# Kernel tuning notes

Measured on AMD Instinct MI355X. Metric: run time of the kernel, lower is better.

The kernel has to match this reference:

```python
import jax, jax.numpy as jnp
import numpy as np

EPS = 1e-5

def _bn(x, g, b):
    # training-mode BatchNorm1d over the batch axis (axis 0), biased variance
    m = jnp.mean(x, axis=0)
    v = jnp.var(x, axis=0)
    return g * (x - m) / jnp.sqrt(v + EPS) + b

def _mlp(x, w1, b1, g1, be1, w2, b2, g2, be2, w3, b3):
    # Linear -> BN -> ReLU -> Linear -> BN -> ReLU -> Linear
    x = jax.nn.relu(_bn(x @ w1.T + b1, g1, be1))
    x = jax.nn.relu(_bn(x @ w2.T + b2, g2, be2))
    return x @ w3.T + b3

def setup_inputs() -> dict:
    key = jax.random.key(0)
    ks = jax.random.split(key, 10)
    B, S, D = 256, 512, 128
    w = lambda k: jax.random.normal(k, (D, D), jnp.float32) * 0.05
    return {
        "s": jax.random.normal(ks[0], (B, S, D), jnp.float32),
        "c": jax.random.normal(ks[1], (B, D), jnp.float32),
        "s_w1": w(ks[2]), "s_b1": jnp.zeros((D,), jnp.float32),
        "s_g1": jnp.ones((D,), jnp.float32), "s_be1": jnp.zeros((D,), jnp.float32),
        "s_w2": w(ks[3]), "s_b2": jnp.zeros((D,), jnp.float32),
        "s_g2": jnp.ones((D,), jnp.float32), "s_be2": jnp.zeros((D,), jnp.float32),
        "s_w3": w(ks[4]), "s_b3": jnp.zeros((D,), jnp.float32),
        "c_w1": w(ks[5]), "c_b1": jnp.zeros((D,), jnp.float32),
        "c_g1": jnp.ones((D,), jnp.float32), "c_be1": jnp.zeros((D,), jnp.float32),
        "c_w2": w(ks[6]), "c_b2": jnp.zeros((D,), jnp.float32),
        "c_g2": jnp.ones((D,), jnp.float32), "c_be2": jnp.zeros((D,), jnp.float32),
        "c_w3": w(ks[7]), "c_b3": jnp.zeros((D,), jnp.float32),
    }

def reference(s, c,
              s_w1, s_b1, s_g1, s_be1, s_w2, s_b2, s_g2, s_be2, s_w3, s_b3,
              c_w1, c_b1, c_g1, c_be1, c_w2, c_b2, c_g2, c_be2, c_w3, c_b3):
    # c_mlp: [B, D] -> [B, D] (BN over batch)
    c_out = _mlp(c, c_w1, c_b1, c_g1, c_be1, c_w2, c_b2, c_g2, c_be2, c_w3, c_b3)
    # s_mlp applied per sequence slice; BN stats over batch axis 0 only
    # (matches the torch loop where each s[:, i, :] gets its own BN stats).
    # s: [B, S, D]; _bn with axis=0 gives per-(slice, feature) stats.
    s_h = _mlp(s, s_w1, s_b1, s_g1, s_be1, s_w2, s_b2, s_g2, s_be2, s_w3, s_b3)
    s_out = s_h * c_out[:, None, :]          # context gate, [B, S, D]
    aggregated_c = jnp.max(s_out, axis=1)    # pooling == 'max', [B, D]
    return (s_out, aggregated_c)
```

## Files before the change

kernel.cpp:

```cpp
#include <hip/hip_runtime.h>
#include <hip/hip_bf16.h>
#include <math.h>

#define BATCH 256
#define SEQ   512
#define DIM   128
#define LDSK  136
#define LDSF  132

typedef __attribute__((ext_vector_type(8))) __bf16  bf16x8;
typedef __attribute__((ext_vector_type(4))) __bf16  bf16x4;
typedef __attribute__((ext_vector_type(4))) float   f32x4;

template<int RT>
__device__ __forceinline__ void matmul_layer(
    const __bf16* __restrict__ Xa, const __bf16* __restrict__ wg,
    const float* bias, f32x4 (&acc)[RT][8], int wave, int m, int q)
{
  const int rowbase = wave * RT * 16;
#pragma unroll
  for (int ct = 0; ct < 8; ++ct) {
    const float b = bias[ct * 16 + m];
    const f32x4 bv = {b, b, b, b};
#pragma unroll
    for (int rt = 0; rt < RT; ++rt) acc[rt][ct] = bv;
  }
#pragma unroll
  for (int ks = 0; ks < 4; ++ks) {
    const int k0 = ks * 32 + q * 8;
    bf16x8 a[RT], bw[8];
#pragma unroll
    for (int rt = 0; rt < RT; ++rt)
      a[rt] = *(const bf16x8*)(Xa + (rowbase + rt * 16 + m) * LDSK + k0);
#pragma unroll
    for (int ct = 0; ct < 8; ++ct)
      bw[ct] = *(const bf16x8*)(wg + (ct * 16 + m) * DIM + k0);
#pragma unroll
    for (int rt = 0; rt < RT; ++rt)
#pragma unroll
      for (int ct = 0; ct < 8; ++ct)
        acc[rt][ct] = __builtin_amdgcn_mfma_f32_16x16x32_bf16(a[rt], bw[ct], acc[rt][ct], 0, 0, 0);
  }
}

template<int RT>
__device__ __forceinline__ void stats_accum(
    const f32x4 (&acc)[RT][8], float* sumL, float* sqL, int m, int q)
{
#pragma unroll
  for (int ct = 0; ct < 8; ++ct) {
    float s = 0.f, ss = 0.f;
#pragma unroll
    for (int rt = 0; rt < RT; ++rt)
#pragma unroll
      for (int r = 0; r < 4; ++r) { const float v = acc[rt][ct][r]; s += v; ss += v * v; }
    s  += __shfl_xor(s, 16, 64);  s  += __shfl_xor(s, 32, 64);
    ss += __shfl_xor(ss, 16, 64); ss += __shfl_xor(ss, 32, 64);
    if (q == 0) { atomicAdd(&sumL[ct * 16 + m], s); atomicAdd(&sqL[ct * 16 + m], ss); }
  }
}

template<int RT>
__device__ __forceinline__ void bn_relu_store(
    const f32x4 (&acc)[RT][8], __bf16* Xa, const float* sumL, const float* sqL,
    const float* g, const float* be, int wave, int m, int q)
{
  const int rowbase = wave * RT * 16;
#pragma unroll
  for (int ct = 0; ct < 8; ++ct) {
    const int n = ct * 16 + m;
    const float mean = sumL[n] * (1.0f / BATCH);
    const float var  = sqL[n]  * (1.0f / BATCH) - mean * mean;
    const float a = g[n] * rsqrtf(var + 1e-5f);
    const float c = be[n] - a * mean;
#pragma unroll
    for (int rt = 0; rt < RT; ++rt)
#pragma unroll
      for (int r = 0; r < 4; ++r) {
        const float y = fmaxf(0.f, a * acc[rt][ct][r] + c);
        const int row = rowbase + rt * 16 + q * 4 + r;
        Xa[row * LDSK + n] = (__bf16)y;
      }
  }
}

template<int NW, bool GATE>
__global__ __launch_bounds__(NW * 64, 2)
void mlp_kernel(const float* __restrict__ xin, long xrow_stride,
                const __bf16* __restrict__ w1, const __bf16* __restrict__ w2,
                const __bf16* __restrict__ w3,
                const float* __restrict__ b1, const float* __restrict__ g1, const float* __restrict__ be1,
                const float* __restrict__ b2, const float* __restrict__ g2, const float* __restrict__ be2,
                const float* __restrict__ b3,
                const float* __restrict__ gate,
                float* __restrict__ out)
{
  const int tid  = threadIdx.x;
  constexpr int NT = NW * 64;
  constexpr int RT = 16 / NW;
  const int wave = tid >> 6, lane = tid & 63;
  const int m = lane & 15, q = lane >> 4;
  const int slice = GATE ? blockIdx.x : 0;
  const float* x0 = GATE ? (xin + (long)slice * DIM) : xin;

  __shared__ __align__(16) char XaRaw[BATCH * LDSK * 2];
  __bf16* Xa = (__bf16*)XaRaw;
  __shared__ float sum1[DIM], sq1[DIM], sum2[DIM], sq2[DIM];
  __shared__ float prm[7 * DIM];

  for (int t = tid; t < DIM; t += NT) { sum1[t] = 0.f; sq1[t] = 0.f; sum2[t] = 0.f; sq2[t] = 0.f; }
  if (tid < DIM) {
    prm[tid]           = b1[tid];  prm[DIM + tid]     = g1[tid];  prm[2 * DIM + tid] = be1[tid];
    prm[3 * DIM + tid] = b2[tid];  prm[4 * DIM + tid] = g2[tid];  prm[5 * DIM + tid] = be2[tid];
    prm[6 * DIM + tid] = b3[tid];
  }

  {
    const int rpi = NT / 32;
    const int r0  = tid >> 5;
    const int c4  = (tid & 31) * 4;
#pragma unroll
    for (int it = 0; it < BATCH / rpi; ++it) {
      const int r = it * rpi + r0;
      const float4 v = *(const float4*)(x0 + (long)r * xrow_stride + c4);
      bf16x4 h = { (__bf16)v.x, (__bf16)v.y, (__bf16)v.z, (__bf16)v.w };
      *(bf16x4*)(Xa + r * LDSK + c4) = h;
    }
  }
  __syncthreads();

  f32x4 acc[RT][8];

  matmul_layer<RT>(Xa, w1, prm, acc, wave, m, q);
  stats_accum<RT>(acc, sum1, sq1, m, q);
  __syncthreads();
  bn_relu_store<RT>(acc, Xa, sum1, sq1, prm + DIM, prm + 2 * DIM, wave, m, q);

  matmul_layer<RT>(Xa, w2, prm + 3 * DIM, acc, wave, m, q);
  stats_accum<RT>(acc, sum2, sq2, m, q);
  __syncthreads();
  bn_relu_store<RT>(acc, Xa, sum2, sq2, prm + 4 * DIM, prm + 5 * DIM, wave, m, q);

  matmul_layer<RT>(Xa, w3, prm + 6 * DIM, acc, wave, m, q);

  if constexpr (GATE) {
    float* Xf = (float*)XaRaw;
    const int c4l = (tid & 31) * 4;
    const int r0  = tid >> 5;
    __syncthreads();
#pragma unroll
    for (int rt = 0; rt < RT; ++rt) {
      float* buf = Xf + (rt & 1) * 64 * LDSF;
#pragma unroll
      for (int ct = 0; ct < 8; ++ct)
#pragma unroll
        for (int r = 0; r < 4; ++r)
          buf[(wave * 16 + q * 4 + r) * LDSF + ct * 16 + m] = acc[rt][ct][r];
      __syncthreads();
#pragma unroll
      for (int it = 0; it < 8; ++it) {
        const int crow = it * 8 + r0;
        const int grow = (crow >> 4) * 64 + rt * 16 + (crow & 15);
        float4 y = *(const float4*)(buf + crow * LDSF + c4l);
        const float4 gv = *(const float4*)(gate + grow * DIM + c4l);
        y.x *= gv.x; y.y *= gv.y; y.z *= gv.z; y.w *= gv.w;
        *(float4*)(out + ((long)grow * SEQ + slice) * DIM + c4l) = y;
      }
    }
  } else {
    const int rowbase = wave * RT * 16;
#pragma unroll
    for (int ct = 0; ct < 8; ++ct) {
      const int col = ct * 16 + m;
#pragma unroll
      for (int rt = 0; rt < RT; ++rt) {
#pragma unroll
        for (int r = 0; r < 4; ++r) {
          const int row = rowbase + rt * 16 + q * 4 + r;
          out[row * DIM + col] = acc[rt][ct][r];
        }
      }
    }
  }
}

__global__ void prep_kernel(const float* __restrict__ w0, const float* __restrict__ w1,
                            const float* __restrict__ w2, const float* __restrict__ w3,
                            const float* __restrict__ w4, const float* __restrict__ w5,
                            __bf16* __restrict__ dst)
{
  const int idx = blockIdx.x * blockDim.x + threadIdx.x;
  const int mi  = idx >> 12;
  const int j   = (idx & 4095) * 4;
  const float* srcs[6] = {w0, w1, w2, w3, w4, w5};
  const float4 v = *(const float4*)(srcs[mi] + j);
  bf16x4 h = { (__bf16)v.x, (__bf16)v.y, (__bf16)v.z, (__bf16)v.w };
  *(bf16x4*)(dst + mi * 16384 + j) = h;
}

__global__ __launch_bounds__(1024) void maxpool_kernel(
    const float* __restrict__ sout, float* __restrict__ agg)
{
  __shared__ float4 red[1024];
  const int b = blockIdx.x;
  const int t = threadIdx.x;
  const int c4 = (t & 31) * 4, rg = t >> 5;
  const float* p = sout + (long)b * SEQ * DIM + c4;
  float4 mx = {-INFINITY, -INFINITY, -INFINITY, -INFINITY};
#pragma unroll 4
  for (int i = rg; i < SEQ; i += 32) {
    const float4 v = *(const float4*)(p + (long)i * DIM);
    mx.x = fmaxf(mx.x, v.x); mx.y = fmaxf(mx.y, v.y);
    mx.z = fmaxf(mx.z, v.z); mx.w = fmaxf(mx.w, v.w);
  }
  red[t] = mx;
  __syncthreads();
  if (t < 32) {
    float4 a = red[t];
#pragma unroll
    for (int k = 1; k < 32; ++k) {
      const float4 v = red[t + 32 * k];
      a.x = fmaxf(a.x, v.x); a.y = fmaxf(a.y, v.y);
      a.z = fmaxf(a.z, v.z); a.w = fmaxf(a.w, v.w);
    }
    *(float4*)(agg + b * DIM + c4) = a;
  }
}

extern "C" void kernel_launch(void* const* d_in, const int* in_sizes, int n_in,
                              void* d_out, int out_size, void* d_ws, size_t ws_size,
                              hipStream_t stream)
{
  const float* s     = (const float*)d_in[0];
  const float* c     = (const float*)d_in[1];
  const float* s_w1  = (const float*)d_in[2];
  const float* s_b1  = (const float*)d_in[3];
  const float* s_g1  = (const float*)d_in[4];
  const float* s_be1 = (const float*)d_in[5];
  const float* s_w2  = (const float*)d_in[6];
  const float* s_b2  = (const float*)d_in[7];
  const float* s_g2  = (const float*)d_in[8];
  const float* s_be2 = (const float*)d_in[9];
  const float* s_w3  = (const float*)d_in[10];
  const float* s_b3  = (const float*)d_in[11];
  const float* c_w1  = (const float*)d_in[12];
  const float* c_b1  = (const float*)d_in[13];
  const float* c_g1  = (const float*)d_in[14];
  const float* c_be1 = (const float*)d_in[15];
  const float* c_w2  = (const float*)d_in[16];
  const float* c_b2  = (const float*)d_in[17];
  const float* c_g2  = (const float*)d_in[18];
  const float* c_be2 = (const float*)d_in[19];
  const float* c_w3  = (const float*)d_in[20];
  const float* c_b3  = (const float*)d_in[21];

  float* out   = (float*)d_out;
  float* c_out = (float*)d_ws;
  __bf16* wbf  = (__bf16*)((char*)d_ws + (size_t)BATCH * DIM * sizeof(float));

  prep_kernel<<<96, 256, 0, stream>>>(s_w1, s_w2, s_w3, c_w1, c_w2, c_w3, wbf);

  mlp_kernel<8, false><<<1, 512, 0, stream>>>(
      c, (long)DIM,
      wbf + 3 * 16384, wbf + 4 * 16384, wbf + 5 * 16384,
      c_b1, c_g1, c_be1, c_b2, c_g2, c_be2, c_b3,
      nullptr, c_out);

  mlp_kernel<4, true><<<SEQ, 256, 0, stream>>>(
      s, (long)SEQ * DIM,
      wbf, wbf + 16384, wbf + 2 * 16384,
      s_b1, s_g1, s_be1, s_b2, s_g2, s_be2, s_b3,
      c_out, out);

  maxpool_kernel<<<BATCH, 1024, 0, stream>>>(out, out + (long)BATCH * SEQ * DIM);
}
```

Measured before the change: 231.4 us.

## Merge weight prep with c-MLP and use 16-wave blocks for s-MLP

```diff
diff --git a/kernel.cpp b/kernel.cpp
--- a/kernel.cpp
+++ b/kernel.cpp
@@ -12,11 +12,13 @@
 typedef __attribute__((ext_vector_type(4))) __bf16  bf16x4;
 typedef __attribute__((ext_vector_type(4))) float   f32x4;
 
-template<int RT>
+template<int RT, bool WF32>
 __device__ __forceinline__ void matmul_layer(
-    const __bf16* __restrict__ Xa, const __bf16* __restrict__ wg,
+    const __bf16* __restrict__ Xa, const void* __restrict__ wg,
     const float* bias, f32x4 (&acc)[RT][8], int wave, int m, int q)
 {
+  const __bf16* wgh = (const __bf16*)wg;
+  const float*  wgf = (const float*)wg;
   const int rowbase = wave * RT * 16;
 #pragma unroll
   for (int ct = 0; ct < 8; ++ct) {
@@ -28,18 +30,32 @@
 #pragma unroll
   for (int ks = 0; ks < 4; ++ks) {
     const int k0 = ks * 32 + q * 8;
-    bf16x8 a[RT], bw[8];
+    bf16x8 a[RT];
 #pragma unroll
     for (int rt = 0; rt < RT; ++rt)
       a[rt] = *(const bf16x8*)(Xa + (rowbase + rt * 16 + m) * LDSK + k0);
 #pragma unroll
-    for (int ct = 0; ct < 8; ++ct)
-      bw[ct] = *(const bf16x8*)(wg + (ct * 16 + m) * DIM + k0);
-#pragma unroll
-    for (int rt = 0; rt < RT; ++rt)
-#pragma unroll
-      for (int ct = 0; ct < 8; ++ct)
-        acc[rt][ct] = __builtin_amdgcn_mfma_f32_16x16x32_bf16(a[rt], bw[ct], acc[rt][ct], 0, 0, 0);
+    for (int cg = 0; cg < 2; ++cg) {
+      bf16x8 bw[4];
+#pragma unroll
+      for (int cj = 0; cj < 4; ++cj) {
+        const int ct = cg * 4 + cj;
+        if constexpr (WF32) {
+          const float4 u0 = *(const float4*)(wgf + (ct * 16 + m) * DIM + k0);
+          const float4 u1 = *(const float4*)(wgf + (ct * 16 + m) * DIM + k0 + 4);
+          bw[cj] = (bf16x8){(__bf16)u0.x, (__bf16)u0.y, (__bf16)u0.z, (__bf16)u0.w,
+                            (__bf16)u1.x, (__bf16)u1.y, (__bf16)u1.z, (__bf16)u1.w};
+        } else {
+          bw[cj] = *(const bf16x8*)(wgh + (ct * 16 + m) * DIM + k0);
+        }
+      }
+#pragma unroll
+      for (int rt = 0; rt < RT; ++rt)
+#pragma unroll
+        for (int cj = 0; cj < 4; ++cj)
+          acc[rt][cg * 4 + cj] =
+              __builtin_amdgcn_mfma_f32_16x16x32_bf16(a[rt], bw[cj], acc[rt][cg * 4 + cj], 0, 0, 0);
+    }
   }
 }
 
@@ -84,24 +100,21 @@
   }
 }
 
-template<int NW, bool GATE>
-__global__ __launch_bounds__(NW * 64, 2)
-void mlp_kernel(const float* __restrict__ xin, long xrow_stride,
-                const __bf16* __restrict__ w1, const __bf16* __restrict__ w2,
-                const __bf16* __restrict__ w3,
-                const float* __restrict__ b1, const float* __restrict__ g1, const float* __restrict__ be1,
-                const float* __restrict__ b2, const float* __restrict__ g2, const float* __restrict__ be2,
-                const float* __restrict__ b3,
-                const float* __restrict__ gate,
-                float* __restrict__ out)
+template<int NW, bool GATE, bool WF32>
+__device__ __forceinline__ void mlp_body(
+    const float* __restrict__ xin, long xrow_stride, int slice,
+    const void* __restrict__ w1, const void* __restrict__ w2, const void* __restrict__ w3,
+    const float* __restrict__ b1, const float* __restrict__ g1, const float* __restrict__ be1,
+    const float* __restrict__ b2, const float* __restrict__ g2, const float* __restrict__ be2,
+    const float* __restrict__ b3,
+    const float* __restrict__ gate, float* __restrict__ out)
 {
   const int tid  = threadIdx.x;
   constexpr int NT = NW * 64;
   constexpr int RT = 16 / NW;
   const int wave = tid >> 6, lane = tid & 63;
   const int m = lane & 15, q = lane >> 4;
-  const int slice = GATE ? blockIdx.x : 0;
-  const float* x0 = GATE ? (xin + (long)slice * DIM) : xin;
+  const float* x0 = xin + (long)slice * (GATE ? DIM : 0);
 
   __shared__ __align__(16) char XaRaw[BATCH * LDSK * 2];
   __bf16* Xa = (__bf16*)XaRaw;
@@ -131,41 +144,45 @@
 
   f32x4 acc[RT][8];
 
-  matmul_layer<RT>(Xa, w1, prm, acc, wave, m, q);
+  matmul_layer<RT, WF32>(Xa, w1, prm, acc, wave, m, q);
   stats_accum<RT>(acc, sum1, sq1, m, q);
   __syncthreads();
   bn_relu_store<RT>(acc, Xa, sum1, sq1, prm + DIM, prm + 2 * DIM, wave, m, q);
 
-  matmul_layer<RT>(Xa, w2, prm + 3 * DIM, acc, wave, m, q);
+  matmul_layer<RT, WF32>(Xa, w2, prm + 3 * DIM, acc, wave, m, q);
   stats_accum<RT>(acc, sum2, sq2, m, q);
   __syncthreads();
   bn_relu_store<RT>(acc, Xa, sum2, sq2, prm + 4 * DIM, prm + 5 * DIM, wave, m, q);
 
-  matmul_layer<RT>(Xa, w3, prm + 6 * DIM, acc, wave, m, q);
+  matmul_layer<RT, WF32>(Xa, w3, prm + 6 * DIM, acc, wave, m, q);
 
   if constexpr (GATE) {
+    static_assert(NW == 16, "gate epilogue assumes NW=16/RT=1");
     float* Xf = (float*)XaRaw;
     const int c4l = (tid & 31) * 4;
     const int r0  = tid >> 5;
     __syncthreads();
 #pragma unroll
-    for (int rt = 0; rt < RT; ++rt) {
-      float* buf = Xf + (rt & 1) * 64 * LDSF;
-#pragma unroll
-      for (int ct = 0; ct < 8; ++ct)
-#pragma unroll
-        for (int r = 0; r < 4; ++r)
-          buf[(wave * 16 + q * 4 + r) * LDSF + ct * 16 + m] = acc[rt][ct][r];
+    for (int ch = 0; ch < 2; ++ch) {
+      if ((wave >> 3) == ch) {
+        const int lr = (wave & 7) * 16 + q * 4;
+#pragma unroll
+        for (int ct = 0; ct < 8; ++ct)
+#pragma unroll
+          for (int r = 0; r < 4; ++r)
+            Xf[(lr + r) * LDSF + ct * 16 + m] = acc[0][ct][r];
+      }
       __syncthreads();
 #pragma unroll
-      for (int it = 0; it < 8; ++it) {
-        const int crow = it * 8 + r0;
-        const int grow = (crow >> 4) * 64 + rt * 16 + (crow & 15);
-        float4 y = *(const float4*)(buf + crow * LDSF + c4l);
+      for (int it = 0; it < 4; ++it) {
+        const int crow = it * 32 + r0;
+        const int grow = ch * 128 + crow;
+        float4 y = *(const float4*)(Xf + crow * LDSF + c4l);
         const float4 gv = *(const float4*)(gate + grow * DIM + c4l);
         y.x *= gv.x; y.y *= gv.y; y.z *= gv.z; y.w *= gv.w;
         *(float4*)(out + ((long)grow * SEQ + slice) * DIM + c4l) = y;
       }
+      if (ch == 0) __syncthreads();
     }
   } else {
     const int rowbase = wave * RT * 16;
@@ -184,18 +201,43 @@
   }
 }
 
-__global__ void prep_kernel(const float* __restrict__ w0, const float* __restrict__ w1,
-                            const float* __restrict__ w2, const float* __restrict__ w3,
-                            const float* __restrict__ w4, const float* __restrict__ w5,
-                            __bf16* __restrict__ dst)
-{
-  const int idx = blockIdx.x * blockDim.x + threadIdx.x;
-  const int mi  = idx >> 12;
-  const int j   = (idx & 4095) * 4;
-  const float* srcs[6] = {w0, w1, w2, w3, w4, w5};
-  const float4 v = *(const float4*)(srcs[mi] + j);
-  bf16x4 h = { (__bf16)v.x, (__bf16)v.y, (__bf16)v.z, (__bf16)v.w };
-  *(bf16x4*)(dst + mi * 16384 + j) = h;
+__global__ __launch_bounds__(1024, 4)
+void s_mlp_kernel(const float* __restrict__ s,
+                  const __bf16* __restrict__ w1, const __bf16* __restrict__ w2,
+                  const __bf16* __restrict__ w3,
+                  const float* __restrict__ b1, const float* __restrict__ g1, const float* __restrict__ be1,
+                  const float* __restrict__ b2, const float* __restrict__ g2, const float* __restrict__ be2,
+                  const float* __restrict__ b3,
+                  const float* __restrict__ gate, float* __restrict__ out)
+{
+  mlp_body<16, true, false>(s, (long)SEQ * DIM, blockIdx.x,
+                            w1, w2, w3, b1, g1, be1, b2, g2, be2, b3, gate, out);
+}
+
+__global__ __launch_bounds__(512, 2)
+void prep_c_kernel(const float* __restrict__ s_w1, const float* __restrict__ s_w2,
+                   const float* __restrict__ s_w3, __bf16* __restrict__ wbf,
+                   const float* __restrict__ c,
+                   const float* __restrict__ c_w1, const float* __restrict__ c_w2,
+                   const float* __restrict__ c_w3,
+                   const float* __restrict__ b1, const float* __restrict__ g1, const float* __restrict__ be1,
+                   const float* __restrict__ b2, const float* __restrict__ g2, const float* __restrict__ be2,
+                   const float* __restrict__ b3,
+                   float* __restrict__ c_out)
+{
+  if (blockIdx.x < 24) {
+    const int idx = blockIdx.x * 512 + threadIdx.x;
+    const int mi  = idx >> 12;
+    const int j   = (idx & 4095) * 4;
+    const float* srcs[3] = {s_w1, s_w2, s_w3};
+    const float4 v = *(const float4*)(srcs[mi] + j);
+    bf16x4 h = { (__bf16)v.x, (__bf16)v.y, (__bf16)v.z, (__bf16)v.w };
+    *(bf16x4*)(wbf + mi * 16384 + j) = h;
+    return;
+  }
+  mlp_body<8, false, true>(c, (long)DIM, 0,
+                           c_w1, c_w2, c_w3, b1, g1, be1, b2, g2, be2, b3,
+                           nullptr, c_out);
 }
 
 __global__ __launch_bounds__(1024) void maxpool_kernel(
@@ -258,17 +300,13 @@
   float* c_out = (float*)d_ws;
   __bf16* wbf  = (__bf16*)((char*)d_ws + (size_t)BATCH * DIM * sizeof(float));
 
-  prep_kernel<<<96, 256, 0, stream>>>(s_w1, s_w2, s_w3, c_w1, c_w2, c_w3, wbf);
-
-  mlp_kernel<8, false><<<1, 512, 0, stream>>>(
-      c, (long)DIM,
-      wbf + 3 * 16384, wbf + 4 * 16384, wbf + 5 * 16384,
-      c_b1, c_g1, c_be1, c_b2, c_g2, c_be2, c_b3,
-      nullptr, c_out);
-
-  mlp_kernel<4, true><<<SEQ, 256, 0, stream>>>(
-      s, (long)SEQ * DIM,
-      wbf, wbf + 16384, wbf + 2 * 16384,
+  prep_c_kernel<<<25, 512, 0, stream>>>(
+      s_w1, s_w2, s_w3, wbf,
+      c, c_w1, c_w2, c_w3,
+      c_b1, c_g1, c_be1, c_b2, c_g2, c_be2, c_b3, c_out);
+
+  s_mlp_kernel<<<SEQ, 1024, 0, stream>>>(
+      s, wbf, wbf + 16384, wbf + 2 * 16384,
       s_b1, s_g1, s_be1, s_b2, s_g2, s_be2, s_b3,
       c_out, out);
 
```

Result: slower. 323.7 us (+39.9%).

## Merge c-MLP into s-MLP launch and move gating into pooling kernel

Applied to the files above, without the earlier changes.

```diff
diff --git a/kernel.cpp b/kernel.cpp
--- a/kernel.cpp
+++ b/kernel.cpp
@@ -84,24 +84,22 @@
   }
 }
 
-template<int NW, bool GATE>
-__global__ __launch_bounds__(NW * 64, 2)
-void mlp_kernel(const float* __restrict__ xin, long xrow_stride,
-                const __bf16* __restrict__ w1, const __bf16* __restrict__ w2,
-                const __bf16* __restrict__ w3,
-                const float* __restrict__ b1, const float* __restrict__ g1, const float* __restrict__ be1,
-                const float* __restrict__ b2, const float* __restrict__ g2, const float* __restrict__ be2,
-                const float* __restrict__ b3,
-                const float* __restrict__ gate,
-                float* __restrict__ out)
-{
+template<int NW>
+__device__ __forceinline__ void mlp_body(
+    const float* __restrict__ x0, long xstride,
+    const __bf16* __restrict__ w1, const __bf16* __restrict__ w2,
+    const __bf16* __restrict__ w3,
+    const float* __restrict__ b1, const float* __restrict__ g1, const float* __restrict__ be1,
+    const float* __restrict__ b2, const float* __restrict__ g2, const float* __restrict__ be2,
+    const float* __restrict__ b3,
+    float* __restrict__ obase, long ostride)
+{
+  static_assert(NW == 4, "epilogue assumes NW=4/RT=4");
   const int tid  = threadIdx.x;
   constexpr int NT = NW * 64;
   constexpr int RT = 16 / NW;
   const int wave = tid >> 6, lane = tid & 63;
   const int m = lane & 15, q = lane >> 4;
-  const int slice = GATE ? blockIdx.x : 0;
-  const float* x0 = GATE ? (xin + (long)slice * DIM) : xin;
 
   __shared__ __align__(16) char XaRaw[BATCH * LDSK * 2];
   __bf16* Xa = (__bf16*)XaRaw;
@@ -122,7 +120,7 @@
 #pragma unroll
     for (int it = 0; it < BATCH / rpi; ++it) {
       const int r = it * rpi + r0;
-      const float4 v = *(const float4*)(x0 + (long)r * xrow_stride + c4);
+      const float4 v = *(const float4*)(x0 + (long)r * xstride + c4);
       bf16x4 h = { (__bf16)v.x, (__bf16)v.y, (__bf16)v.z, (__bf16)v.w };
       *(bf16x4*)(Xa + r * LDSK + c4) = h;
     }
@@ -143,7 +141,7 @@
 
   matmul_layer<RT>(Xa, w3, prm + 6 * DIM, acc, wave, m, q);
 
-  if constexpr (GATE) {
+  {
     float* Xf = (float*)XaRaw;
     const int c4l = (tid & 31) * 4;
     const int r0  = tid >> 5;
@@ -161,27 +159,37 @@
       for (int it = 0; it < 8; ++it) {
         const int crow = it * 8 + r0;
         const int grow = (crow >> 4) * 64 + rt * 16 + (crow & 15);
-        float4 y = *(const float4*)(buf + crow * LDSF + c4l);
-        const float4 gv = *(const float4*)(gate + grow * DIM + c4l);
-        y.x *= gv.x; y.y *= gv.y; y.z *= gv.z; y.w *= gv.w;
-        *(float4*)(out + ((long)grow * SEQ + slice) * DIM + c4l) = y;
+        const float4 y = *(const float4*)(buf + crow * LDSF + c4l);
+        *(float4*)(obase + (long)grow * ostride + c4l) = y;
       }
     }
-  } else {
-    const int rowbase = wave * RT * 16;
-#pragma unroll
-    for (int ct = 0; ct < 8; ++ct) {
-      const int col = ct * 16 + m;
-#pragma unroll
-      for (int rt = 0; rt < RT; ++rt) {
-#pragma unroll
-        for (int r = 0; r < 4; ++r) {
-          const int row = rowbase + rt * 16 + q * 4 + r;
-          out[row * DIM + col] = acc[rt][ct][r];
-        }
-      }
-    }
-  }
+  }
+}
+
+__global__ __launch_bounds__(256, 2)
+void mlp_all_kernel(const float* __restrict__ s, const float* __restrict__ c,
+                    const __bf16* __restrict__ wbf,
+                    const float* __restrict__ s_b1, const float* __restrict__ s_g1, const float* __restrict__ s_be1,
+                    const float* __restrict__ s_b2, const float* __restrict__ s_g2, const float* __restrict__ s_be2,
+                    const float* __restrict__ s_b3,
+                    const float* __restrict__ c_b1, const float* __restrict__ c_g1, const float* __restrict__ c_be1,
+                    const float* __restrict__ c_b2, const float* __restrict__ c_g2, const float* __restrict__ c_be2,
+                    const float* __restrict__ c_b3,
+                    float* __restrict__ out, float* __restrict__ c_out)
+{
+  const int bid = blockIdx.x;
+  const bool isC = (bid == SEQ);
+  const float* x0     = isC ? c : (s + (long)bid * DIM);
+  const long   xs     = isC ? (long)DIM : (long)SEQ * DIM;
+  float*       ob     = isC ? c_out : (out + (long)bid * DIM);
+  const long   os     = isC ? (long)DIM : (long)SEQ * DIM;
+  const __bf16* w1 = wbf + (isC ? 3 : 0) * 16384;
+  const __bf16* w2 = wbf + (isC ? 4 : 1) * 16384;
+  const __bf16* w3 = wbf + (isC ? 5 : 2) * 16384;
+  mlp_body<4>(x0, xs, w1, w2, w3,
+              isC ? c_b1 : s_b1, isC ? c_g1 : s_g1, isC ? c_be1 : s_be1,
+              isC ? c_b2 : s_b2, isC ? c_g2 : s_g2, isC ? c_be2 : s_be2,
+              isC ? c_b3 : s_b3, ob, os);
 }
 
 __global__ void prep_kernel(const float* __restrict__ w0, const float* __restrict__ w1,
@@ -198,18 +206,21 @@
   *(bf16x4*)(dst + mi * 16384 + j) = h;
 }
 
-__global__ __launch_bounds__(1024) void maxpool_kernel(
-    const float* __restrict__ sout, float* __restrict__ agg)
+__global__ __launch_bounds__(1024) void gatepool_kernel(
+    float* __restrict__ sout, const float* __restrict__ c_out, float* __restrict__ agg)
 {
   __shared__ float4 red[1024];
   const int b = blockIdx.x;
   const int t = threadIdx.x;
   const int c4 = (t & 31) * 4, rg = t >> 5;
-  const float* p = sout + (long)b * SEQ * DIM + c4;
+  float* p = sout + (long)b * SEQ * DIM + c4;
+  const float4 gv = *(const float4*)(c_out + b * DIM + c4);
   float4 mx = {-INFINITY, -INFINITY, -INFINITY, -INFINITY};
 #pragma unroll 4
   for (int i = rg; i < SEQ; i += 32) {
-    const float4 v = *(const float4*)(p + (long)i * DIM);
+    float4 v = *(const float4*)(p + (long)i * DIM);
+    v.x *= gv.x; v.y *= gv.y; v.z *= gv.z; v.w *= gv.w;
+    *(float4*)(p + (long)i * DIM) = v;
     mx.x = fmaxf(mx.x, v.x); mx.y = fmaxf(mx.y, v.y);
     mx.z = fmaxf(mx.z, v.z); mx.w = fmaxf(mx.w, v.w);
   }
@@ -223,7 +234,7 @@
       a.x = fmaxf(a.x, v.x); a.y = fmaxf(a.y, v.y);
       a.z = fmaxf(a.z, v.z); a.w = fmaxf(a.w, v.w);
     }
-    *(float4*)(agg + b * DIM + c4) = a;
+    *(float4*)(agg + b * DIM + t * 4) = a;
   }
 }
 
@@ -260,17 +271,11 @@
 
   prep_kernel<<<96, 256, 0, stream>>>(s_w1, s_w2, s_w3, c_w1, c_w2, c_w3, wbf);
 
-  mlp_kernel<8, false><<<1, 512, 0, stream>>>(
-      c, (long)DIM,
-      wbf + 3 * 16384, wbf + 4 * 16384, wbf + 5 * 16384,
+  mlp_all_kernel<<<SEQ + 1, 256, 0, stream>>>(
+      s, c, wbf,
+      s_b1, s_g1, s_be1, s_b2, s_g2, s_be2, s_b3,
       c_b1, c_g1, c_be1, c_b2, c_g2, c_be2, c_b3,
-      nullptr, c_out);
-
-  mlp_kernel<4, true><<<SEQ, 256, 0, stream>>>(
-      s, (long)SEQ * DIM,
-      wbf, wbf + 16384, wbf + 2 * 16384,
-      s_b1, s_g1, s_be1, s_b2, s_g2, s_be2, s_b3,
-      c_out, out);
-
-  maxpool_kernel<<<BATCH, 1024, 0, stream>>>(out, out + (long)BATCH * SEQ * DIM);
-}
+      out, c_out);
+
+  gatepool_kernel<<<BATCH, 1024, 0, stream>>>(out, c_out, out + (long)BATCH * SEQ * DIM);
+}
```

Result: no change. 234.3 us (+1.2%).
